# Kernel tuning notes

Hardware: AMD Instinct MI355X
Metric: run time of the kernel (lower is better)

Reference implementation:

```python
import jax, jax.numpy as jnp
import numpy as np

D_MODEL = 2048
N_HEADS = 16
HEAD_DIM = D_MODEL // N_HEADS
SCALE = HEAD_DIM ** -0.5


def setup_inputs() -> dict:
    key = jax.random.key(0)
    ks = jax.random.split(key, 9)
    B, L, D = 4, 4096, D_MODEL
    s = 1.0 / np.sqrt(D)
    inp = {"x": jax.random.normal(ks[0], (B, L, D), dtype=jnp.float32)}
    inp["Wq"] = jax.random.normal(ks[1], (D, D), dtype=jnp.float32) * s
    inp["bq"] = jnp.zeros((D,), dtype=jnp.float32)
    inp["Wk"] = jax.random.normal(ks[2], (D, D), dtype=jnp.float32) * s
    inp["bk"] = jnp.zeros((D,), dtype=jnp.float32)
    inp["Wv"] = jax.random.normal(ks[3], (D, D), dtype=jnp.float32) * s
    inp["bv"] = jnp.zeros((D,), dtype=jnp.float32)
    inp["Wo"] = jax.random.normal(ks[4], (D, D), dtype=jnp.float32) * s
    inp["bo"] = jnp.zeros((D,), dtype=jnp.float32)
    return inp


def reference(x, Wq, bq, Wk, bk, Wv, bv, Wo, bo):
    B, L, D = x.shape
    H, Hd = N_HEADS, HEAD_DIM
    # projections (torch Linear: x @ W.T + b)
    q = jnp.einsum('bld,ed->ble', x, Wq) + bq
    k = jnp.einsum('bld,ed->ble', x, Wk) + bk
    v = jnp.einsum('bld,ed->ble', x, Wv) + bv
    phi_q = jax.nn.elu(q) + 1.0
    phi_k = jax.nn.elu(k) + 1.0
    # (B, L, H, Hd)
    phi_q = phi_q.reshape(B, L, H, Hd)
    phi_k = phi_k.reshape(B, L, H, Hd)
    v = v.reshape(B, L, H, Hd)
    # elementwise prefix sum over sequence dim
    kv_sum = jnp.cumsum(phi_k * v, axis=1)  # (B, L, H, Hd)
    context = (phi_q * kv_sum).reshape(B, L, D) * SCALE
    return jnp.einsum('bld,ed->ble', context, Wo) + bo
```

## Files before the change

kernel.cpp:

```cpp
#include <hip/hip_runtime.h>
#include <hip/hip_bf16.h>
#include <cstdint>
#include <cstddef>

typedef __bf16 bf16x8 __attribute__((ext_vector_type(8)));
typedef __bf16 bf16x4 __attribute__((ext_vector_type(4)));
typedef float  f32x4  __attribute__((ext_vector_type(4)));

#define D_MODEL 2048
#define SEQ     4096
#define BATCH   4
#define M_TOK   (BATCH * SEQ)
#define ATTN_SCALE 0.08838834764831845f

#define BM 128
#define BN 128
#define BK 32

#define NSEG   64
#define SEGLEN (SEQ / NSEG)

__device__ __forceinline__ void async_load16(const void* g, void* l) {
    __builtin_amdgcn_global_load_lds(
        (const __attribute__((address_space(1))) unsigned int*)g,
        (__attribute__((address_space(3))) unsigned int*)l,
        16, 0, 0);
}

__global__ __launch_bounds__(256) void k_cast_bf16(const float* __restrict__ in,
                                                   __bf16* __restrict__ out,
                                                   int n8) {
    int i = blockIdx.x * 256 + threadIdx.x;
    if (i >= n8) return;
    const float4* in4 = (const float4*)in;
    float4 a = in4[2 * i];
    float4 b = in4[2 * i + 1];
    bf16x8 o;
    o[0] = (__bf16)a.x; o[1] = (__bf16)a.y; o[2] = (__bf16)a.z; o[3] = (__bf16)a.w;
    o[4] = (__bf16)b.x; o[5] = (__bf16)b.y; o[6] = (__bf16)b.z; o[7] = (__bf16)b.w;
    ((bf16x8*)out)[i] = o;
}

template <int PHI, typename OUT_T>
__device__ __forceinline__ void gemm_bt(const __bf16* __restrict__ A,
                                        const __bf16* __restrict__ Bm,
                                        const float* __restrict__ bias,
                                        OUT_T* __restrict__ C,
                                        int K, int N) {
    __shared__ __align__(16) __bf16 As[BM * BK];
    __shared__ __align__(16) __bf16 Bs[BN * BK];

    const int tid  = threadIdx.x;
    const int lane = tid & 63;
    const int wave = tid >> 6;
    const int waveM = wave & 1;
    const int waveN = wave >> 1;
    const long bm = (long)blockIdx.y * BM;
    const long bn = (long)blockIdx.x * BN;

    const __bf16* ga0 = A  + (bm + (tid >> 2)) * (long)K + (tid & 3) * 8;
    const __bf16* ga1 = ga0 + 64L * K;
    const __bf16* gb0 = Bm + (bn + (tid >> 2)) * (long)K + (tid & 3) * 8;
    const __bf16* gb1 = gb0 + 64L * K;
    __bf16* la0 = As + tid * 8;
    __bf16* la1 = As + 2048 + tid * 8;
    __bf16* lb0 = Bs + tid * 8;
    __bf16* lb1 = Bs + 2048 + tid * 8;

    const int mrow = waveM * 64 + (lane & 15);
    const int nrow = waveN * 64 + (lane & 15);
    const int kq   = (lane >> 4) * 8;

    f32x4 acc[4][4] = {};

    for (int k0 = 0; k0 < K; k0 += BK) {
        async_load16(ga0 + k0, la0);
        async_load16(ga1 + k0, la1);
        async_load16(gb0 + k0, lb0);
        async_load16(gb1 + k0, lb1);
        __syncthreads();

        bf16x8 af[4], bfr[4];
#pragma unroll
        for (int i = 0; i < 4; i++)
            af[i] = *(const bf16x8*)(As + (mrow + i * 16) * BK + kq);
#pragma unroll
        for (int j = 0; j < 4; j++)
            bfr[j] = *(const bf16x8*)(Bs + (nrow + j * 16) * BK + kq);
#pragma unroll
        for (int i = 0; i < 4; i++)
#pragma unroll
            for (int j = 0; j < 4; j++)
                acc[i][j] = __builtin_amdgcn_mfma_f32_16x16x32_bf16(
                    af[i], bfr[j], acc[i][j], 0, 0, 0);
        __syncthreads();
    }

    const int r0 = (lane >> 4) * 4;
    const int cn = lane & 15;
#pragma unroll
    for (int i = 0; i < 4; i++) {
        long mg = bm + waveM * 64 + i * 16 + r0;
#pragma unroll
        for (int j = 0; j < 4; j++) {
            long ng = bn + waveN * 64 + j * 16 + cn;
            float bia = bias[ng];
#pragma unroll
            for (int r = 0; r < 4; r++) {
                float v = acc[i][j][r] + bia;
                if (PHI) v = (v > 0.f) ? (v + 1.f) : __expf(v);
                C[(mg + r) * (long)N + ng] = (OUT_T)v;
            }
        }
    }
}

__global__ __launch_bounds__(256) void k_gemm_qkv(
    const __bf16* __restrict__ xb,
    const __bf16* __restrict__ wq, const __bf16* __restrict__ wk, const __bf16* __restrict__ wv,
    const float* __restrict__ bq, const float* __restrict__ bk, const float* __restrict__ bv,
    __bf16* __restrict__ oq, __bf16* __restrict__ ok, __bf16* __restrict__ ov) {
    const int z = blockIdx.z;
    const __bf16* W = (z == 0) ? wq : (z == 1) ? wk : wv;
    const float*  b = (z == 0) ? bq : (z == 1) ? bk : bv;
    __bf16*       o = (z == 0) ? oq : (z == 1) ? ok : ov;
    if (z < 2)
        gemm_bt<1, __bf16>(xb, W, b, o, D_MODEL, D_MODEL);
    else
        gemm_bt<0, __bf16>(xb, W, b, o, D_MODEL, D_MODEL);
}

__global__ __launch_bounds__(256) void k_gemm_out(
    const __bf16* __restrict__ ctx, const __bf16* __restrict__ wo,
    const float* __restrict__ bo, float* __restrict__ out) {
    gemm_bt<0, float>(ctx, wo, bo, out, D_MODEL, D_MODEL);
}

__global__ __launch_bounds__(256) void k_scan_partial(
    const __bf16* __restrict__ phik, const __bf16* __restrict__ v,
    float* __restrict__ partial) {
    const int b  = blockIdx.z;
    const int s  = blockIdx.y;
    const int c0 = blockIdx.x * 1024 + threadIdx.x * 4;
    long base = ((long)b * SEQ + (long)s * SEGLEN) * D_MODEL + c0;
    const bf16x4* pk = (const bf16x4*)(phik + base);
    const bf16x4* pv = (const bf16x4*)(v + base);
    float s0 = 0, s1 = 0, s2 = 0, s3 = 0;
    for (int l = 0; l < SEGLEN; l++) {
        bf16x4 a = *pk, w = *pv;
        s0 += (float)a[0] * (float)w[0];
        s1 += (float)a[1] * (float)w[1];
        s2 += (float)a[2] * (float)w[2];
        s3 += (float)a[3] * (float)w[3];
        pk += D_MODEL / 4; pv += D_MODEL / 4;
    }
    *(float4*)(partial + ((long)(b * NSEG + s)) * D_MODEL + c0) = make_float4(s0, s1, s2, s3);
}

__global__ __launch_bounds__(256) void k_scan_apply(
    const __bf16* __restrict__ phiq,
    __bf16* phik_ctx,
    const __bf16* __restrict__ v,
    const float* __restrict__ partial) {
    const int b  = blockIdx.z;
    const int s  = blockIdx.y;
    const int c0 = blockIdx.x * 1024 + threadIdx.x * 4;
    float r0 = 0, r1 = 0, r2 = 0, r3 = 0;
    for (int sp = 0; sp < s; sp++) {
        float4 p = *(const float4*)(partial + ((long)(b * NSEG + sp)) * D_MODEL + c0);
        r0 += p.x; r1 += p.y; r2 += p.z; r3 += p.w;
    }
    long base = ((long)b * SEQ + (long)s * SEGLEN) * D_MODEL + c0;
    bf16x4* pk = (bf16x4*)(phik_ctx + base);
    const bf16x4* pv = (const bf16x4*)(v + base);
    const bf16x4* pq = (const bf16x4*)(phiq + base);
    for (int l = 0; l < SEGLEN; l++) {
        bf16x4 a = *pk, w = *pv, q = *pq;
        r0 += (float)a[0] * (float)w[0];
        r1 += (float)a[1] * (float)w[1];
        r2 += (float)a[2] * (float)w[2];
        r3 += (float)a[3] * (float)w[3];
        bf16x4 o;
        o[0] = (__bf16)((float)q[0] * r0 * ATTN_SCALE);
        o[1] = (__bf16)((float)q[1] * r1 * ATTN_SCALE);
        o[2] = (__bf16)((float)q[2] * r2 * ATTN_SCALE);
        o[3] = (__bf16)((float)q[3] * r3 * ATTN_SCALE);
        *pk = o;
        pk += D_MODEL / 4; pv += D_MODEL / 4; pq += D_MODEL / 4;
    }
}

extern "C" void kernel_launch(void* const* d_in, const int* in_sizes, int n_in,
                              void* d_out, int out_size, void* d_ws, size_t ws_size,
                              hipStream_t stream) {
    const float* x  = (const float*)d_in[0];
    const float* Wq = (const float*)d_in[1];
    const float* bq = (const float*)d_in[2];
    const float* Wk = (const float*)d_in[3];
    const float* bk = (const float*)d_in[4];
    const float* Wv = (const float*)d_in[5];
    const float* bv = (const float*)d_in[6];
    const float* Wo = (const float*)d_in[7];
    const float* bo = (const float*)d_in[8];

    const size_t XB = (size_t)M_TOK * D_MODEL;
    const size_t WB = (size_t)D_MODEL * D_MODEL;

    char* p = (char*)d_ws;
    __bf16* xb   = (__bf16*)p; p += XB * 2;
    __bf16* wqb  = (__bf16*)p; p += WB * 2;
    __bf16* wkb  = (__bf16*)p; p += WB * 2;
    __bf16* wvb  = (__bf16*)p; p += WB * 2;
    __bf16* wob  = (__bf16*)p; p += WB * 2;
    __bf16* phiq = (__bf16*)p; p += XB * 2;
    __bf16* phik = (__bf16*)p; p += XB * 2;
    __bf16* vb   = (__bf16*)p; p += XB * 2;
    if ((size_t)(p - (char*)d_ws) > ws_size) return;

    float*  partial = (float*)xb;
    __bf16* ctx     = phik;

    k_cast_bf16<<<dim3((unsigned)(XB / 8 / 256)), 256, 0, stream>>>(x, xb, (int)(XB / 8));
    k_cast_bf16<<<dim3((unsigned)(WB / 8 / 256)), 256, 0, stream>>>(Wq, wqb, (int)(WB / 8));
    k_cast_bf16<<<dim3((unsigned)(WB / 8 / 256)), 256, 0, stream>>>(Wk, wkb, (int)(WB / 8));
    k_cast_bf16<<<dim3((unsigned)(WB / 8 / 256)), 256, 0, stream>>>(Wv, wvb, (int)(WB / 8));
    k_cast_bf16<<<dim3((unsigned)(WB / 8 / 256)), 256, 0, stream>>>(Wo, wob, (int)(WB / 8));

    k_gemm_qkv<<<dim3(D_MODEL / BN, M_TOK / BM, 3), 256, 0, stream>>>(
        xb, wqb, wkb, wvb, bq, bk, bv, phiq, phik, vb);

    k_scan_partial<<<dim3(2, NSEG, BATCH), 256, 0, stream>>>(phik, vb, partial);
    k_scan_apply<<<dim3(2, NSEG, BATCH), 256, 0, stream>>>(phiq, phik, vb, partial);

    k_gemm_out<<<dim3(D_MODEL / BN, M_TOK / BM, 1), 256, 0, stream>>>(
        ctx, wob, bo, (float*)d_out);
}
```

Measured before the change: 991.5 us.

## Double GEMM K-tile to 64 with XOR-swizzled LDS, merge weight casts

```diff
diff --git a/kernel.cpp b/kernel.cpp
--- a/kernel.cpp
+++ b/kernel.cpp
@@ -15,7 +15,7 @@
 
 #define BM 128
 #define BN 128
-#define BK 32
+#define BK 64
 
 #define NSEG   64
 #define SEGLEN (SEQ / NSEG)
@@ -41,6 +41,25 @@
     ((bf16x8*)out)[i] = o;
 }
 
+__global__ __launch_bounds__(256) void k_cast_w4(const float* __restrict__ w0,
+                                                 const float* __restrict__ w1,
+                                                 const float* __restrict__ w2,
+                                                 const float* __restrict__ w3,
+                                                 __bf16* __restrict__ out, int n8) {
+    const float* srcs[4] = {w0, w1, w2, w3};
+    const float* in = srcs[blockIdx.y];
+    __bf16* o = out + (size_t)blockIdx.y * (size_t)n8 * 8;
+    int i = blockIdx.x * 256 + threadIdx.x;
+    if (i >= n8) return;
+    const float4* in4 = (const float4*)in;
+    float4 a = in4[2 * i];
+    float4 b = in4[2 * i + 1];
+    bf16x8 v;
+    v[0] = (__bf16)a.x; v[1] = (__bf16)a.y; v[2] = (__bf16)a.z; v[3] = (__bf16)a.w;
+    v[4] = (__bf16)b.x; v[5] = (__bf16)b.y; v[6] = (__bf16)b.z; v[7] = (__bf16)b.w;
+    ((bf16x8*)o)[i] = v;
+}
+
 template <int PHI, typename OUT_T>
 __device__ __forceinline__ void gemm_bt(const __bf16* __restrict__ A,
                                         const __bf16* __restrict__ Bm,
@@ -58,41 +77,55 @@
     const long bm = (long)blockIdx.y * BM;
     const long bn = (long)blockIdx.x * BN;
 
-    const __bf16* ga0 = A  + (bm + (tid >> 2)) * (long)K + (tid & 3) * 8;
-    const __bf16* ga1 = ga0 + 64L * K;
-    const __bf16* gb0 = Bm + (bn + (tid >> 2)) * (long)K + (tid & 3) * 8;
-    const __bf16* gb1 = gb0 + 64L * K;
-    __bf16* la0 = As + tid * 8;
-    __bf16* la1 = As + 2048 + tid * 8;
-    __bf16* lb0 = Bs + tid * 8;
-    __bf16* lb1 = Bs + 2048 + tid * 8;
+    const int srow  = tid >> 3;
+    const int sphys = tid & 7;
+    const __bf16* gA[4]; const __bf16* gB[4];
+    __bf16* lA[4]; __bf16* lB[4];
+#pragma unroll
+    for (int q = 0; q < 4; q++) {
+        int r  = q * 32 + srow;
+        int cb = (sphys ^ (r & 7)) * 8;
+        gA[q] = A  + (bm + r) * (long)K + cb;
+        gB[q] = Bm + (bn + r) * (long)K + cb;
+        lA[q] = As + q * 2048 + tid * 8;
+        lB[q] = Bs + q * 2048 + tid * 8;
+    }
 
     const int mrow = waveM * 64 + (lane & 15);
     const int nrow = waveN * 64 + (lane & 15);
-    const int kq   = (lane >> 4) * 8;
+    const int ksel = lane >> 4;
 
     f32x4 acc[4][4] = {};
 
     for (int k0 = 0; k0 < K; k0 += BK) {
-        async_load16(ga0 + k0, la0);
-        async_load16(ga1 + k0, la1);
-        async_load16(gb0 + k0, lb0);
-        async_load16(gb1 + k0, lb1);
+#pragma unroll
+        for (int q = 0; q < 4; q++) async_load16(gA[q] + k0, lA[q]);
+#pragma unroll
+        for (int q = 0; q < 4; q++) async_load16(gB[q] + k0, lB[q]);
         __syncthreads();
 
-        bf16x8 af[4], bfr[4];
-#pragma unroll
-        for (int i = 0; i < 4; i++)
-            af[i] = *(const bf16x8*)(As + (mrow + i * 16) * BK + kq);
-#pragma unroll
-        for (int j = 0; j < 4; j++)
-            bfr[j] = *(const bf16x8*)(Bs + (nrow + j * 16) * BK + kq);
-#pragma unroll
-        for (int i = 0; i < 4; i++)
-#pragma unroll
-            for (int j = 0; j < 4; j++)
-                acc[i][j] = __builtin_amdgcn_mfma_f32_16x16x32_bf16(
-                    af[i], bfr[j], acc[i][j], 0, 0, 0);
+#pragma unroll
+        for (int s = 0; s < 2; s++) {
+            bf16x8 af[4], bfr[4];
+#pragma unroll
+            for (int i = 0; i < 4; i++) {
+                int r = mrow + i * 16;
+                int p = (s * 4 + ksel) ^ (r & 7);
+                af[i] = *(const bf16x8*)(As + r * 64 + p * 8);
+            }
+#pragma unroll
+            for (int j = 0; j < 4; j++) {
+                int r = nrow + j * 16;
+                int p = (s * 4 + ksel) ^ (r & 7);
+                bfr[j] = *(const bf16x8*)(Bs + r * 64 + p * 8);
+            }
+#pragma unroll
+            for (int i = 0; i < 4; i++)
+#pragma unroll
+                for (int j = 0; j < 4; j++)
+                    acc[i][j] = __builtin_amdgcn_mfma_f32_16x16x32_bf16(
+                        af[i], bfr[j], acc[i][j], 0, 0, 0);
+        }
         __syncthreads();
     }
 
@@ -221,10 +254,7 @@
     __bf16* ctx     = phik;
 
     k_cast_bf16<<<dim3((unsigned)(XB / 8 / 256)), 256, 0, stream>>>(x, xb, (int)(XB / 8));
-    k_cast_bf16<<<dim3((unsigned)(WB / 8 / 256)), 256, 0, stream>>>(Wq, wqb, (int)(WB / 8));
-    k_cast_bf16<<<dim3((unsigned)(WB / 8 / 256)), 256, 0, stream>>>(Wk, wkb, (int)(WB / 8));
-    k_cast_bf16<<<dim3((unsigned)(WB / 8 / 256)), 256, 0, stream>>>(Wv, wvb, (int)(WB / 8));
-    k_cast_bf16<<<dim3((unsigned)(WB / 8 / 256)), 256, 0, stream>>>(Wo, wob, (int)(WB / 8));
+    k_cast_w4<<<dim3((unsigned)(WB / 8 / 256), 4), 256, 0, stream>>>(Wq, Wk, Wv, Wo, wqb, (int)(WB / 8));
 
     k_gemm_qkv<<<dim3(D_MODEL / BN, M_TOK / BM, 3), 256, 0, stream>>>(
         xb, wqb, wkb, wvb, bq, bk, bv, phiq, phik, vb);
```

After: 928.9 us. 6.3% less time.
